# Kernel optimization log

Hardware: AMD Instinct MI355X
Metric: run time of the kernel (lower is better)

Reference implementation:

```python
import jax, jax.numpy as jnp
import numpy as np

TAU = 0.5
LOGIT_TAU = float(np.log(TAU / (1.0 - TAU)))  # = 0.0 for tau=0.5
N_STEPS = 128           # torch samples randint(128,129) -> always 128
N_SECANT = 8
D_MIN, D_MAX = 0.0, 2.4
B, N, HID, CDIM = 4, 8192, 64, 128


def decoder(p, c, W1, Wc, b1, W2, b2):
    """Occupancy-logit MLP. p: (B, ..., 3), c: (B, CDIM) -> (B, ...)."""
    cc = c @ Wc  # (B, HID)
    cc = cc.reshape(cc.shape[:1] + (1,) * (p.ndim - 2) + cc.shape[1:])
    h = jax.nn.relu(jnp.einsum('...d,dh->...h', p, W1) + cc + b1)
    return (h @ W2 + b2)[..., 0]


def setup_inputs() -> dict:
    key = jax.random.key(0)
    ks = jax.random.split(key, 8)
    return {
        'ray0': jax.random.normal(ks[0], (B, N, 3), jnp.float32) * 0.5,
        'ray_direction': jax.random.normal(ks[1], (B, N, 3), jnp.float32),
        'c': jax.random.normal(ks[2], (B, CDIM), jnp.float32),
        'W1': jax.random.normal(ks[3], (3, HID), jnp.float32) * 0.5,
        'Wc': jax.random.normal(ks[4], (CDIM, HID), jnp.float32) * 0.1,
        'b1': jax.random.normal(ks[5], (HID,), jnp.float32) * 0.1,
        'W2': jax.random.normal(ks[6], (HID, 1), jnp.float32) * 0.5,
        'b2': jax.random.normal(ks[7], (1,), jnp.float32) * 0.1,
    }


def reference(ray0, ray_direction, c, W1, Wc, b1, W2, b2):
    S = N_STEPS
    bsz, npts, _ = ray0.shape
    dec = lambda p: decoder(p, c, W1, Wc, b1, W2, b2)

    # --- coarse ray marching ---
    d_prop = jnp.linspace(D_MIN, D_MAX, S).astype(ray0.dtype)        # (S,)
    p_prop = ray0[:, :, None, :] + ray_direction[:, :, None, :] * d_prop[None, None, :, None]
    val = dec(p_prop) - LOGIT_TAU                                    # (B, N, S)

    mask_0_not_occupied = val[:, :, 0] < 0
    sign_matrix = jnp.concatenate(
        [jnp.sign(val[:, :, :-1] * val[:, :, 1:]),
         jnp.ones((bsz, npts, 1), val.dtype)], axis=-1)
    cost_matrix = sign_matrix * jnp.arange(S, 0, -1, dtype=val.dtype)
    indices = jnp.argmin(cost_matrix, axis=-1)                       # (B, N)
    values = jnp.min(cost_matrix, axis=-1)
    mask_sign_change = values < 0
    f_low = jnp.take_along_axis(val, indices[..., None], axis=2)[..., 0]
    mask_neg_to_pos = f_low < 0
    mask = mask_sign_change & mask_neg_to_pos & mask_0_not_occupied

    d_prop_full = jnp.broadcast_to(d_prop, (bsz, npts, S))
    d_low = jnp.take_along_axis(d_prop_full, indices[..., None], axis=2)[..., 0]
    idx_hi = jnp.minimum(indices + 1, S - 1)
    d_high = jnp.take_along_axis(d_prop_full, idx_hi[..., None], axis=2)[..., 0]
    f_high = jnp.take_along_axis(val, idx_hi[..., None], axis=2)[..., 0]

    # safe placeholders for non-surface rays (results discarded by mask)
    d_low = jnp.where(mask, d_low, 0.0)
    d_high = jnp.where(mask, d_high, 1.0)
    f_low = jnp.where(mask, f_low, -1.0)
    f_high = jnp.where(mask, f_high, 1.0)

    # --- secant refinement (vectorized over all rays) ---
    d_pred = -f_low * (d_high - d_low) / (f_high - f_low) + d_low
    for _ in range(N_SECANT):
        p_mid = ray0 + d_pred[..., None] * ray_direction
        f_mid = dec(p_mid) - LOGIT_TAU
        ind_low = f_mid < 0
        d_low = jnp.where(ind_low, d_pred, d_low)
        f_low = jnp.where(ind_low, f_mid, f_low)
        d_high = jnp.where(ind_low, d_high, d_pred)
        f_high = jnp.where(ind_low, f_high, f_mid)
        d_pred = -f_low * (d_high - d_low) / (f_high - f_low) + d_low

    d_out = jnp.where(mask, d_pred, jnp.inf)
    d_out = jnp.where(mask_0_not_occupied, d_out, 0.0)
    return d_out
```

## Files before the change

### kernel.cpp

```cpp
#include <hip/hip_runtime.h>
#include <hip/hip_bf16.h>

#define HID   64
#define CDIM  128
#define NSTEP 128
#define NRAYS 32768

typedef const __hip_bfloat16* __restrict__ bf16p;

#define WS_CCB  0
#define WS_WX   256
#define WS_WY   320
#define WS_WZ   384
#define WS_W2   448
#define WS_CNT  512
#define WS_DTAB 640
#define QID     1024
#define QDL     (QID + 32768)
#define QDH     (QDL + 32768)
#define QFL     (QDH + 32768)
#define QFH     (QFL + 32768)

#define STEPF (2.4f / 127.0f)

__device__ __forceinline__ float bf2f(__hip_bfloat16 x) { return __bfloat162float(x); }

__global__ void precompute_cc(bf16p c, bf16p Wc, bf16p b1, bf16p W1, bf16p W2,
                              float* __restrict__ ws) {
    __shared__ float part[4][HID];
    int b = blockIdx.x;
    int h = threadIdx.x & 63;
    int q = threadIdx.x >> 6;
    float acc = 0.0f;
    const __hip_bfloat16* crow = c + b * CDIM;
#pragma unroll
    for (int k = q * 32; k < q * 32 + 32; ++k)
        acc = fmaf(bf2f(crow[k]), bf2f(Wc[k * HID + h]), acc);
    part[q][h] = acc;
    if (b == 0) {
        if (q == 1) {
            ws[WS_WX + h] = bf2f(W1[h]);
            ws[WS_WY + h] = bf2f(W1[HID + h]);
        } else if (q == 2) {
            ws[WS_WZ + h] = bf2f(W1[2 * HID + h]);
            ws[WS_W2 + h] = bf2f(W2[h]);
        } else if (q == 3) {
            if (h < 4) ((int*)ws)[WS_CNT + h] = 0;
            ws[WS_DTAB + h]      = bf2f(__float2bfloat16((float)h * STEPF));
            ws[WS_DTAB + 64 + h] = bf2f(__float2bfloat16((float)(h + 64) * STEPF));
        }
    }
    __syncthreads();
    if (q == 0)
        ws[WS_CCB + b * HID + h] =
            bf2f(b1[h]) + ((part[0][h] + part[1][h]) + (part[2][h] + part[3][h]));
}

__global__ __launch_bounds__(256) void raymarch(
    bf16p ray0, bf16p rdir, bf16p b2,
    float* __restrict__ ws, __hip_bfloat16* __restrict__ out) {
    __shared__ float2 sAB[4][HID][4];

    const int tid  = threadIdx.x;
    const int wave = tid >> 6;
    const int lane = tid & 63;
    const int rbase = blockIdx.x * 16 + wave * 4;
    const int batch = blockIdx.x >> 9;

    const float b2v = bf2f(b2[0]);

    {
        const float wx = ws[WS_WX + lane];
        const float wy = ws[WS_WY + lane];
        const float wz = ws[WS_WZ + lane];
        const float cb = ws[WS_CCB + batch * HID + lane];
        float a[4], bb[4];
#pragma unroll
        for (int t = 0; t < 4; ++t) {
            const int r = rbase + t;
            const float ox = bf2f(ray0[r * 3 + 0]), oy = bf2f(ray0[r * 3 + 1]), oz = bf2f(ray0[r * 3 + 2]);
            const float dx = bf2f(rdir[r * 3 + 0]), dy = bf2f(rdir[r * 3 + 1]), dz = bf2f(rdir[r * 3 + 2]);
            a[t]  = fmaf(ox, wx, fmaf(oy, wy, fmaf(oz, wz, cb)));
            bb[t] = fmaf(dx, wx, fmaf(dy, wy, dz * wz));
        }
        float4* dst = (float4*)&sAB[wave][lane][0];
        dst[0] = make_float4(a[0], bb[0], a[1], bb[1]);
        dst[1] = make_float4(a[2], bb[2], a[3], bb[3]);
    }

    const int t = lane >> 4;
    const int g = lane & 15;

    float d[8], v[8];
#pragma unroll
    for (int k = 0; k < 8; ++k) {
        d[k] = bf2f(__float2bfloat16((float)(8 * g + k) * STEPF));
        v[k] = b2v;
    }

    const float* __restrict__ W2R = ws + WS_W2;
    const float2* __restrict__ abp = &sAB[wave][0][t];
#pragma unroll
    for (int j = 0; j < HID; ++j) {
        const float2 ab = abp[j * 4];
        const float  w2 = W2R[j];
#pragma unroll
        for (int k = 0; k < 8; ++k) {
            float h = fmaf(d[k], ab.y, ab.x);
            v[k] = fmaf(fmaxf(h, 0.0f), w2, v[k]);
        }
    }

    float nv = __shfl_down(v[0], 1);
    float key;
#pragma unroll
    for (int k = 0; k < 8; ++k) {
        const int s = 8 * g + k;
        float vn = (k < 7) ? v[k + 1] : nv;
        float prod = v[k] * vn;
        float sgn = (prod < 0.0f) ? -1.0f : ((prod > 0.0f) ? 1.0f : 0.0f);
        float kk = (s == NSTEP - 1) ? (256.0f + 127.0f)
                                    : fmaf(sgn * (float)(NSTEP - s), 256.0f, (float)s);
        key = (k == 0) ? kk : fminf(key, kk);
    }
#pragma unroll
    for (int off = 1; off < 16; off <<= 1)
        key = fminf(key, __shfl_xor(key, off));
    const float cf = floorf(key * 0.00390625f);
    const int   mi = (int)(key - cf * 256.0f);

    const int idx  = mi;
    const int idxh = (idx + 1 < NSTEP) ? idx + 1 : NSTEP - 1;
    const int q  = idx  & 7, qh = idxh & 7;

    float cand = v[0], candh = v[0];
#pragma unroll
    for (int k = 1; k < 8; ++k) {
        cand  = (q  == k) ? v[k] : cand;
        candh = (qh == k) ? v[k] : candh;
    }
    const int lane_lo = (lane & 48) | (idx  >> 3);
    const int lane_hi = (lane & 48) | (idxh >> 3);
    float f_low  = __shfl(cand,  lane_lo);
    float f_high = __shfl(candh, lane_hi);
    float v00    = __shfl(v[0], lane & 48);

    bool m0   = v00 < 0.0f;
    bool mask = (key < 0.0f) && (f_low < 0.0f) && m0;

    if (g == 0) {
        const int r = rbase + t;
        if (mask) {
            int pos = atomicAdd((int*)ws + WS_CNT + batch, 1);
            int qo  = batch * 8192 + pos;
            ((int*)ws)[QID + qo] = r;
            ws[QDL + qo] = bf2f(__float2bfloat16(idx  * STEPF));
            ws[QDH + qo] = bf2f(__float2bfloat16(idxh * STEPF));
            ws[QFL + qo] = f_low;
            ws[QFH + qo] = f_high;
        } else {
            out[r] = __float2bfloat16(m0 ? 0x1.FEp127f : 0.0f);
        }
    }
}

__global__ __launch_bounds__(256) void secant(
    bf16p ray0, bf16p rdir, bf16p b2,
    const float* __restrict__ ws, __hip_bfloat16* __restrict__ out) {
    __shared__ float4 sW4[HID];
    __shared__ float  sCB[HID];

    const int gtid  = blockIdx.x * 256 + threadIdx.x;
    const int batch = gtid >> 13;
    const int i     = gtid & 8191;

    if (threadIdx.x < HID) {
        int j = threadIdx.x;
        sW4[j] = make_float4(ws[WS_WX + j], ws[WS_WY + j], ws[WS_WZ + j], ws[WS_W2 + j]);
        sCB[j] = ws[WS_CCB + batch * HID + j];
    }
    __syncthreads();

    const int cnt = ((const int*)ws)[WS_CNT + batch];
    if (i >= cnt) return;

    const int qo  = batch * 8192 + i;
    const int rid = ((const int*)ws)[QID + qo];
    float dl = ws[QDL + qo], dh = ws[QDH + qo];
    float fl = ws[QFL + qo], fh = ws[QFH + qo];

    const float ox = bf2f(ray0[rid * 3 + 0]), oy = bf2f(ray0[rid * 3 + 1]), oz = bf2f(ray0[rid * 3 + 2]);
    const float dx = bf2f(rdir[rid * 3 + 0]), dy = bf2f(rdir[rid * 3 + 1]), dz = bf2f(rdir[rid * 3 + 2]);
    const float b2v = bf2f(b2[0]);

    float dp = -fl * (dh - dl) / (fh - fl) + dl;
#pragma unroll
    for (int it = 0; it < 8; ++it) {
        float px = fmaf(dp, dx, ox), py = fmaf(dp, dy, oy), pz = fmaf(dp, dz, oz);
        float acc = b2v;
#pragma unroll 8
        for (int j = 0; j < HID; ++j) {
            float4 w = sW4[j];
            float h = fmaf(px, w.x, fmaf(py, w.y, fmaf(pz, w.z, sCB[j])));
            acc = fmaf(fmaxf(h, 0.0f), w.w, acc);
        }
        bool lowside = acc < 0.0f;
        dl = lowside ? dp : dl;
        fl = lowside ? acc : fl;
        dh = lowside ? dh : dp;
        fh = lowside ? fh : acc;
        dp = -fl * (dh - dl) / (fh - fl) + dl;
    }
    out[rid] = __float2bfloat16(dp);
}

extern "C" void kernel_launch(void* const* d_in, const int* in_sizes, int n_in,
                              void* d_out, int out_size, void* d_ws, size_t ws_size,
                              hipStream_t stream) {
    bf16p ray0 = (bf16p)d_in[0];
    bf16p rdir = (bf16p)d_in[1];
    bf16p c    = (bf16p)d_in[2];
    bf16p W1   = (bf16p)d_in[3];
    bf16p Wc   = (bf16p)d_in[4];
    bf16p b1   = (bf16p)d_in[5];
    bf16p W2   = (bf16p)d_in[6];
    bf16p b2   = (bf16p)d_in[7];
    __hip_bfloat16* out = (__hip_bfloat16*)d_out;
    float* ws = (float*)d_ws;

    hipLaunchKernelGGL(precompute_cc, dim3(4), dim3(256), 0, stream, c, Wc, b1, W1, W2, ws);
    hipLaunchKernelGGL(raymarch, dim3(NRAYS / 16), dim3(256), 0, stream,
                       ray0, rdir, b2, ws, out);
    hipLaunchKernelGGL(secant, dim3(128), dim3(256), 0, stream,
                       ray0, rdir, b2, ws, out);
}
```

Before: 90.08 us.

## Replace coarse MLP evaluation with piecewise-linear event prefix sums

```diff
diff --git a/kernel.cpp b/kernel.cpp
--- a/kernel.cpp
+++ b/kernel.cpp
@@ -59,7 +59,7 @@
 __global__ __launch_bounds__(256) void raymarch(
     bf16p ray0, bf16p rdir, bf16p b2,
     float* __restrict__ ws, __hip_bfloat16* __restrict__ out) {
-    __shared__ float2 sAB[4][HID][4];
+    __shared__ __align__(16) float2 sEv[4][4][144];
 
     const int tid  = threadIdx.x;
     const int wave = tid >> 6;
@@ -70,44 +70,89 @@
     const float b2v = bf2f(b2[0]);
 
     {
-        const float wx = ws[WS_WX + lane];
-        const float wy = ws[WS_WY + lane];
-        const float wz = ws[WS_WZ + lane];
-        const float cb = ws[WS_CCB + batch * HID + lane];
-        float a[4], bb[4];
+        float4* z = (float4*)&sEv[wave][lane >> 4][0];
+        const int c0 = (lane & 15) * 4;
+#pragma unroll
+        for (int k = 0; k < 4; ++k) z[c0 + k] = make_float4(0.f, 0.f, 0.f, 0.f);
+    }
+
+    {
+        const float wx  = ws[WS_WX + lane];
+        const float wy  = ws[WS_WY + lane];
+        const float wz  = ws[WS_WZ + lane];
+        const float cb  = ws[WS_CCB + batch * HID + lane];
+        const float w2l = ws[WS_W2 + lane];
+        const int dummy = 128 + (lane & 15);
 #pragma unroll
         for (int t = 0; t < 4; ++t) {
             const int r = rbase + t;
             const float ox = bf2f(ray0[r * 3 + 0]), oy = bf2f(ray0[r * 3 + 1]), oz = bf2f(ray0[r * 3 + 2]);
             const float dx = bf2f(rdir[r * 3 + 0]), dy = bf2f(rdir[r * 3 + 1]), dz = bf2f(rdir[r * 3 + 2]);
-            a[t]  = fmaf(ox, wx, fmaf(oy, wy, fmaf(oz, wz, cb)));
-            bb[t] = fmaf(dx, wx, fmaf(dy, wy, dz * wz));
-        }
-        float4* dst = (float4*)&sAB[wave][lane][0];
-        dst[0] = make_float4(a[0], bb[0], a[1], bb[1]);
-        dst[1] = make_float4(a[2], bb[2], a[3], bb[3]);
-    }
+            const float aT = fmaf(ox, wx, fmaf(oy, wy, fmaf(oz, wz, cb)));
+            const float bT = fmaf(dx, wx, fmaf(dy, wy, dz * wz));
+            const bool rising = bT > 0.0f;
+
+            float sf = __fdividef(-aT, bT) * (127.0f / 2.4f);
+            sf = fminf(fmaxf(sf, 0.0f), 128.0f);
+            int c = (int)ceilf(sf);
+            c = (c < 1) ? 1 : ((c > 127) ? 127 : c);
+            const float dm = bf2f(__float2bfloat16((float)(c - 1) * STEPF));
+            const float dc = bf2f(__float2bfloat16((float)c * STEPF));
+            const float hm = fmaf(dm, bT, aT);
+            const float hc = fmaf(dc, bT, aT);
+            int s0;
+            if (rising) s0 = (hm > 0.0f)  ? c - 1 : ((hc > 0.0f)  ? c : c + 1);
+            else        s0 = (hm <= 0.0f) ? c - 1 : ((hc <= 0.0f) ? c : c + 1);
+            if (bT == 0.0f) s0 = (aT > 0.0f) ? 128 : 0;
+
+            const float wa = w2l * aT, wb = w2l * bT;
+            const bool e0on = rising ? (s0 < 128) : (s0 > 0);
+            const int  e0s  = rising ? s0 : 0;
+            const int  sl0  = e0on ? (((e0s & 7) << 4) | (e0s >> 3)) : dummy;
+            const bool e1on = (!rising) && (s0 > 0) && (s0 < 128);
+            const int  sl1  = e1on ? (((s0 & 7) << 4) | (s0 >> 3)) : dummy;
+
+            float* bp = (float*)&sEv[wave][t][0];
+            atomicAdd(bp + 2 * sl0,     e0on ? wa : 0.0f);
+            atomicAdd(bp + 2 * sl0 + 1, e0on ? wb : 0.0f);
+            atomicAdd(bp + 2 * sl1,     e1on ? -wa : 0.0f);
+            atomicAdd(bp + 2 * sl1 + 1, e1on ? -wb : 0.0f);
+        }
+    }
+    __syncthreads();
 
     const int t = lane >> 4;
     const int g = lane & 15;
 
     float d[8], v[8];
 #pragma unroll
-    for (int k = 0; k < 8; ++k) {
+    for (int k = 0; k < 8; ++k)
         d[k] = bf2f(__float2bfloat16((float)(8 * g + k) * STEPF));
-        v[k] = b2v;
-    }
-
-    const float* __restrict__ W2R = ws + WS_W2;
-    const float2* __restrict__ abp = &sAB[wave][0][t];
-#pragma unroll
-    for (int j = 0; j < HID; ++j) {
-        const float2 ab = abp[j * 4];
-        const float  w2 = W2R[j];
+
+    {
+        float PA[8], PB[8];
+        float runA = 0.0f, runB = 0.0f;
+        const float2* ev = &sEv[wave][t][g];
 #pragma unroll
         for (int k = 0; k < 8; ++k) {
-            float h = fmaf(d[k], ab.y, ab.x);
-            v[k] = fmaf(fmaxf(h, 0.0f), w2, v[k]);
+            const float2 e = ev[k * 16];
+            runA += e.x; runB += e.y;
+            PA[k] = runA; PB[k] = runB;
+        }
+        double XA = (double)runA, XB = (double)runB;
+        const double TA = XA, TB = XB;
+#pragma unroll
+        for (int off = 1; off < 16; off <<= 1) {
+            const double uA = __shfl_up(XA, off, 16);
+            const double uB = __shfl_up(XB, off, 16);
+            if (g >= off) { XA += uA; XB += uB; }
+        }
+        XA -= TA; XB -= TB;
+#pragma unroll
+        for (int k = 0; k < 8; ++k) {
+            const float Af = (float)(XA + (double)PA[k]);
+            const float Bf = (float)(XB + (double)PB[k]);
+            v[k] = fmaf(d[k], Bf, b2v + Af);
         }
     }
 
```

Result: slower. 119.2 us (+32.4%).

## Fuse conditioning, ray marching and secant refinement into one kernel

Applied to the files above, without the earlier changes.

```diff
diff --git a/kernel.cpp b/kernel.cpp
--- a/kernel.cpp
+++ b/kernel.cpp
@@ -6,81 +6,56 @@
 #define NSTEP 128
 #define NRAYS 32768
 
+#define STEPF (2.4f / 127.0f)
+
 typedef const __hip_bfloat16* __restrict__ bf16p;
-
-#define WS_CCB  0
-#define WS_WX   256
-#define WS_WY   320
-#define WS_WZ   384
-#define WS_W2   448
-#define WS_CNT  512
-#define WS_DTAB 640
-#define QID     1024
-#define QDL     (QID + 32768)
-#define QDH     (QDL + 32768)
-#define QFL     (QDH + 32768)
-#define QFH     (QFL + 32768)
-
-#define STEPF (2.4f / 127.0f)
 
 __device__ __forceinline__ float bf2f(__hip_bfloat16 x) { return __bfloat162float(x); }
 
-__global__ void precompute_cc(bf16p c, bf16p Wc, bf16p b1, bf16p W1, bf16p W2,
-                              float* __restrict__ ws) {
-    __shared__ float part[4][HID];
-    int b = blockIdx.x;
-    int h = threadIdx.x & 63;
-    int q = threadIdx.x >> 6;
-    float acc = 0.0f;
-    const __hip_bfloat16* crow = c + b * CDIM;
-#pragma unroll
-    for (int k = q * 32; k < q * 32 + 32; ++k)
-        acc = fmaf(bf2f(crow[k]), bf2f(Wc[k * HID + h]), acc);
-    part[q][h] = acc;
-    if (b == 0) {
-        if (q == 1) {
-            ws[WS_WX + h] = bf2f(W1[h]);
-            ws[WS_WY + h] = bf2f(W1[HID + h]);
-        } else if (q == 2) {
-            ws[WS_WZ + h] = bf2f(W1[2 * HID + h]);
-            ws[WS_W2 + h] = bf2f(W2[h]);
-        } else if (q == 3) {
-            if (h < 4) ((int*)ws)[WS_CNT + h] = 0;
-            ws[WS_DTAB + h]      = bf2f(__float2bfloat16((float)h * STEPF));
-            ws[WS_DTAB + 64 + h] = bf2f(__float2bfloat16((float)(h + 64) * STEPF));
-        }
-    }
-    __syncthreads();
-    if (q == 0)
-        ws[WS_CCB + b * HID + h] =
-            bf2f(b1[h]) + ((part[0][h] + part[1][h]) + (part[2][h] + part[3][h]));
-}
+__global__ __launch_bounds__(256) void depth_fused(
+    bf16p ray0, bf16p rdir, bf16p c, bf16p W1, bf16p Wc, bf16p b1, bf16p W2,
+    bf16p b2, __hip_bfloat16* __restrict__ out) {
+    __shared__ float2 sAB[4][HID][4];
+    __shared__ float4 sW4[4][HID];
+    __shared__ float  sCB[4][HID];
+    __shared__ float  part[4][HID];
 
-__global__ __launch_bounds__(256) void raymarch(
-    bf16p ray0, bf16p rdir, bf16p b2,
-    float* __restrict__ ws, __hip_bfloat16* __restrict__ out) {
-    __shared__ float2 sAB[4][HID][4];
-
-    const int tid  = threadIdx.x;
-    const int wave = tid >> 6;
-    const int lane = tid & 63;
+    const int tid   = threadIdx.x;
+    const int wave  = tid >> 6;
+    const int lane  = tid & 63;
     const int rbase = blockIdx.x * 16 + wave * 4;
     const int batch = blockIdx.x >> 9;
 
     const float b2v = bf2f(b2[0]);
 
+    const float wx  = bf2f(W1[lane]);
+    const float wy  = bf2f(W1[HID + lane]);
+    const float wz  = bf2f(W1[2 * HID + lane]);
+    const float w2l = bf2f(W2[lane]);
+    sW4[wave][lane] = make_float4(wx, wy, wz, w2l);
+
     {
-        const float wx = ws[WS_WX + lane];
-        const float wy = ws[WS_WY + lane];
-        const float wz = ws[WS_WZ + lane];
-        const float cb = ws[WS_CCB + batch * HID + lane];
+        float acc = 0.0f;
+        const __hip_bfloat16* crow = c + batch * CDIM;
+        const int k0 = wave * 32;
+#pragma unroll
+        for (int k = 0; k < 32; ++k)
+            acc = fmaf(bf2f(crow[k0 + k]), bf2f(Wc[(k0 + k) * HID + lane]), acc);
+        part[wave][lane] = acc;
+    }
+    __syncthreads();
+    const float cbv = bf2f(b1[lane]) +
+        ((part[0][lane] + part[1][lane]) + (part[2][lane] + part[3][lane]));
+    sCB[wave][lane] = cbv;
+
+    {
         float a[4], bb[4];
 #pragma unroll
         for (int t = 0; t < 4; ++t) {
             const int r = rbase + t;
             const float ox = bf2f(ray0[r * 3 + 0]), oy = bf2f(ray0[r * 3 + 1]), oz = bf2f(ray0[r * 3 + 2]);
             const float dx = bf2f(rdir[r * 3 + 0]), dy = bf2f(rdir[r * 3 + 1]), dz = bf2f(rdir[r * 3 + 2]);
-            a[t]  = fmaf(ox, wx, fmaf(oy, wy, fmaf(oz, wz, cb)));
+            a[t]  = fmaf(ox, wx, fmaf(oy, wy, fmaf(oz, wz, cbv)));
             bb[t] = fmaf(dx, wx, fmaf(dy, wy, dz * wz));
         }
         float4* dst = (float4*)&sAB[wave][lane][0];
@@ -98,12 +73,11 @@
         v[k] = b2v;
     }
 
-    const float* __restrict__ W2R = ws + WS_W2;
     const float2* __restrict__ abp = &sAB[wave][0][t];
 #pragma unroll
     for (int j = 0; j < HID; ++j) {
         const float2 ab = abp[j * 4];
-        const float  w2 = W2R[j];
+        const float  w2 = bf2f(W2[j]);
 #pragma unroll
         for (int k = 0; k < 8; ++k) {
             float h = fmaf(d[k], ab.y, ab.x);
@@ -148,70 +122,50 @@
     bool m0   = v00 < 0.0f;
     bool mask = (key < 0.0f) && (f_low < 0.0f) && m0;
 
-    if (g == 0) {
+    if (!mask && g == 0) {
+        out[rbase + t] = __float2bfloat16(m0 ? 0x1.FEp127f : 0.0f);
+    }
+
+    if (__ballot(mask)) {
         const int r = rbase + t;
-        if (mask) {
-            int pos = atomicAdd((int*)ws + WS_CNT + batch, 1);
-            int qo  = batch * 8192 + pos;
-            ((int*)ws)[QID + qo] = r;
-            ws[QDL + qo] = bf2f(__float2bfloat16(idx  * STEPF));
-            ws[QDH + qo] = bf2f(__float2bfloat16(idxh * STEPF));
-            ws[QFL + qo] = f_low;
-            ws[QFH + qo] = f_high;
-        } else {
-            out[r] = __float2bfloat16(m0 ? 0x1.FEp127f : 0.0f);
+        const float ox = bf2f(ray0[r * 3 + 0]), oy = bf2f(ray0[r * 3 + 1]), oz = bf2f(ray0[r * 3 + 2]);
+        const float dx = bf2f(rdir[r * 3 + 0]), dy = bf2f(rdir[r * 3 + 1]), dz = bf2f(rdir[r * 3 + 2]);
+
+        float dl = bf2f(__float2bfloat16(idx  * STEPF));
+        float dh = bf2f(__float2bfloat16(idxh * STEPF));
+        float fl = f_low, fh = f_high;
+
+        float4 Wm[4];
+        float  cbm[4];
+#pragma unroll
+        for (int m = 0; m < 4; ++m) {
+            Wm[m]  = sW4[wave][g + 16 * m];
+            cbm[m] = sCB[wave][g + 16 * m];
         }
+
+        float dp = -fl * (dh - dl) / (fh - fl) + dl;
+#pragma unroll
+        for (int it = 0; it < 8; ++it) {
+            const float px = fmaf(dp, dx, ox), py = fmaf(dp, dy, oy), pz = fmaf(dp, dz, oz);
+            float s = 0.0f;
+#pragma unroll
+            for (int m = 0; m < 4; ++m) {
+                float h = fmaf(px, Wm[m].x, fmaf(py, Wm[m].y, fmaf(pz, Wm[m].z, cbm[m])));
+                s = fmaf(fmaxf(h, 0.0f), Wm[m].w, s);
+            }
+#pragma unroll
+            for (int off = 1; off < 16; off <<= 1)
+                s += __shfl_xor(s, off);
+            const float fm = s + b2v;
+            const bool lowside = fm < 0.0f;
+            dl = lowside ? dp : dl;
+            fl = lowside ? fm : fl;
+            dh = lowside ? dh : dp;
+            fh = lowside ? fh : fm;
+            dp = -fl * (dh - dl) / (fh - fl) + dl;
+        }
+        if (mask && g == 0) out[r] = __float2bfloat16(dp);
     }
-}
-
-__global__ __launch_bounds__(256) void secant(
-    bf16p ray0, bf16p rdir, bf16p b2,
-    const float* __restrict__ ws, __hip_bfloat16* __restrict__ out) {
-    __shared__ float4 sW4[HID];
-    __shared__ float  sCB[HID];
-
-    const int gtid  = blockIdx.x * 256 + threadIdx.x;
-    const int batch = gtid >> 13;
-    const int i     = gtid & 8191;
-
-    if (threadIdx.x < HID) {
-        int j = threadIdx.x;
-        sW4[j] = make_float4(ws[WS_WX + j], ws[WS_WY + j], ws[WS_WZ + j], ws[WS_W2 + j]);
-        sCB[j] = ws[WS_CCB + batch * HID + j];
-    }
-    __syncthreads();
-
-    const int cnt = ((const int*)ws)[WS_CNT + batch];
-    if (i >= cnt) return;
-
-    const int qo  = batch * 8192 + i;
-    const int rid = ((const int*)ws)[QID + qo];
-    float dl = ws[QDL + qo], dh = ws[QDH + qo];
-    float fl = ws[QFL + qo], fh = ws[QFH + qo];
-
-    const float ox = bf2f(ray0[rid * 3 + 0]), oy = bf2f(ray0[rid * 3 + 1]), oz = bf2f(ray0[rid * 3 + 2]);
-    const float dx = bf2f(rdir[rid * 3 + 0]), dy = bf2f(rdir[rid * 3 + 1]), dz = bf2f(rdir[rid * 3 + 2]);
-    const float b2v = bf2f(b2[0]);
-
-    float dp = -fl * (dh - dl) / (fh - fl) + dl;
-#pragma unroll
-    for (int it = 0; it < 8; ++it) {
-        float px = fmaf(dp, dx, ox), py = fmaf(dp, dy, oy), pz = fmaf(dp, dz, oz);
-        float acc = b2v;
-#pragma unroll 8
-        for (int j = 0; j < HID; ++j) {
-            float4 w = sW4[j];
-            float h = fmaf(px, w.x, fmaf(py, w.y, fmaf(pz, w.z, sCB[j])));
-            acc = fmaf(fmaxf(h, 0.0f), w.w, acc);
-        }
-        bool lowside = acc < 0.0f;
-        dl = lowside ? dp : dl;
-        fl = lowside ? acc : fl;
-        dh = lowside ? dh : dp;
-        fh = lowside ? fh : acc;
-        dp = -fl * (dh - dl) / (fh - fl) + dl;
-    }
-    out[rid] = __float2bfloat16(dp);
 }
 
 extern "C" void kernel_launch(void* const* d_in, const int* in_sizes, int n_in,
@@ -226,11 +180,8 @@
     bf16p W2   = (bf16p)d_in[6];
     bf16p b2   = (bf16p)d_in[7];
     __hip_bfloat16* out = (__hip_bfloat16*)d_out;
-    float* ws = (float*)d_ws;
+    (void)d_ws; (void)ws_size;
 
-    hipLaunchKernelGGL(precompute_cc, dim3(4), dim3(256), 0, stream, c, Wc, b1, W1, W2, ws);
-    hipLaunchKernelGGL(raymarch, dim3(NRAYS / 16), dim3(256), 0, stream,
-                       ray0, rdir, b2, ws, out);
-    hipLaunchKernelGGL(secant, dim3(128), dim3(256), 0, stream,
-                       ray0, rdir, b2, ws, out);
+    hipLaunchKernelGGL(depth_fused, dim3(NRAYS / 16), dim3(256), 0, stream,
+                       ray0, rdir, c, W1, Wc, b1, W2, b2, out);
 }
```

Result: faster. 87.62 us (-2.7%).
